# Kernel tuning notes

Hardware: AMD Instinct MI355X
Metric: run time of the kernel (lower is better)

Reference implementation:

```python
import jax, jax.numpy as jnp
import numpy as np

N_BRANCH, N_LAYER = 4, 3
B, T, D_IN = 4, 1024, 32
D_MODEL, D_INNER, D_STATE, D_CONV, DT_RANK = 128, 256, 16, 4, 8
EMBED = 64
MAX_NORM = 10.0  # safe_expmap0 tangent-norm clip
EPS = 1e-7


def setup_inputs() -> dict:
    key = jax.random.key(0)
    ks = jax.random.split(key, 12)
    def nrm(k, shp, s=0.02):
        return s * jax.random.normal(k, shp, dtype=jnp.float32)
    A_init = jnp.log(jnp.arange(1, D_STATE + 1, dtype=jnp.float32))
    return {
        "trend": jax.random.normal(ks[0], (B, T, D_IN), jnp.float32),
        "seasonal_coarse": jax.random.normal(ks[1], (B, T, D_IN), jnp.float32),
        "seasonal_fine": jax.random.normal(ks[2], (B, T, D_IN), jnp.float32),
        "residual": jax.random.normal(ks[3], (B, T, D_IN), jnp.float32),
        "W_ip": nrm(ks[4], (N_BRANCH, D_IN, D_MODEL)),
        "b_ip": jnp.zeros((N_BRANCH, D_MODEL), jnp.float32),
        "W_in": nrm(ks[5], (N_BRANCH, N_LAYER, D_MODEL, 2 * D_INNER)),
        "conv_w": nrm(ks[6], (N_BRANCH, N_LAYER, D_INNER, D_CONV), 0.1),
        "conv_b": jnp.zeros((N_BRANCH, N_LAYER, D_INNER), jnp.float32),
        "W_x": nrm(ks[7], (N_BRANCH, N_LAYER, D_INNER, DT_RANK + 2 * D_STATE)),
        "W_dt": nrm(ks[8], (N_BRANCH, N_LAYER, DT_RANK, D_INNER), 0.1),
        "b_dt": jnp.full((N_BRANCH, N_LAYER, D_INNER), -4.6, jnp.float32),  # softplus ~ 0.01
        "A_log": jnp.broadcast_to(A_init, (N_BRANCH, N_LAYER, D_INNER, D_STATE)),
        "D_param": jnp.ones((N_BRANCH, N_LAYER, D_INNER), jnp.float32),
        "W_out": nrm(ks[9], (N_BRANCH, N_LAYER, D_INNER, D_MODEL)),
        "W_op": nrm(ks[10], (N_BRANCH, D_MODEL, EMBED)),
        "b_op": jnp.zeros((N_BRANCH, EMBED), jnp.float32),
        "eff_scale": jnp.asarray(0.1, jnp.float32),
    }


def _mamba_layer(x, Win, cw, cb, Wx, Wdt, bdt, Alog, Dp, Wout):
    # x: [B, T, d_model]
    Tlen = x.shape[1]
    xz = x @ Win                                   # [B,T,2*di]
    xp, z = jnp.split(xz, 2, axis=-1)
    # causal depthwise conv1d, kernel D_CONV
    xpad = jnp.pad(xp, ((0, 0), (D_CONV - 1, 0), (0, 0)))
    xc = sum(xpad[:, k:k + Tlen, :] * cw[:, k] for k in range(D_CONV))
    xc = jax.nn.silu(xc + cb)                      # [B,T,di]
    dbl = xc @ Wx                                  # [B,T,r+2s]
    dt = jax.nn.softplus(dbl[..., :DT_RANK] @ Wdt + bdt)   # [B,T,di]
    Bm = dbl[..., DT_RANK:DT_RANK + D_STATE]       # [B,T,s]
    Cm = dbl[..., DT_RANK + D_STATE:]              # [B,T,s]
    A = -jnp.exp(Alog)                             # [di,s]
    dA = jnp.exp(dt[..., None] * A)                # [B,T,di,s]
    dBx = (dt * xc)[..., None] * Bm[:, :, None, :] # [B,T,di,s]

    def step(h, inp):
        dA_t, dBx_t, C_t = inp
        h = dA_t * h + dBx_t
        return h, jnp.einsum('bds,bs->bd', h, C_t)

    h0 = jnp.zeros((x.shape[0], D_INNER, D_STATE), x.dtype)
    _, ys = jax.lax.scan(step, h0, (jnp.swapaxes(dA, 0, 1),
                                     jnp.swapaxes(dBx, 0, 1),
                                     jnp.swapaxes(Cm, 0, 1)))
    y = jnp.swapaxes(ys, 0, 1) + Dp * xc
    return (y * jax.nn.silu(z)) @ Wout


def _embed(x, Wip, bip, Wins, cws, cbs, Wxs, Wdts, bdts, Alogs, Dps, Wouts, Wop, bop):
    h = x @ Wip + bip
    for l in range(N_LAYER):
        h = _mamba_layer(h, Wins[l], cws[l], cbs[l], Wxs[l], Wdts[l], bdts[l],
                         Alogs[l], Dps[l], Wouts[l])
    return h.mean(axis=1) @ Wop + bop              # [B, EMBED]


def _expmap0(v):
    # safe expmap0 on Lorentz (k=1): clip tangent norm at MAX_NORM
    n = jnp.linalg.norm(v, axis=-1, keepdims=True)
    nc = jnp.clip(n, EPS, MAX_NORM)
    v = v * (nc / jnp.maximum(n, EPS))
    return jnp.concatenate([jnp.cosh(nc), jnp.sinh(nc) / nc * v], axis=-1)


def _projx(x):
    sp = x[..., 1:]
    t = jnp.sqrt(1.0 + jnp.sum(sp * sp, axis=-1, keepdims=True))
    return jnp.concatenate([t, sp], axis=-1)


def _logmap0(x):
    sp = x[..., 1:]
    t = jnp.maximum(x[..., :1], 1.0 + EPS)
    d = jnp.arccosh(t)
    spn = jnp.maximum(jnp.linalg.norm(sp, axis=-1, keepdims=True), EPS)
    return d * sp / spn


def _forward(trend, seasonal_coarse, seasonal_fine, residual,
             W_ip, b_ip, W_in, conv_w, conv_b, W_x, W_dt, b_dt,
             A_log, D_param, W_out, W_op, b_op, eff_scale):
    xs = [trend, seasonal_coarse, seasonal_fine, residual]
    z_t = [
        _embed(xs[b], W_ip[b], b_ip[b], W_in[b], conv_w[b], conv_b[b], W_x[b],
               W_dt[b], b_dt[b], A_log[b], D_param[b], W_out[b], W_op[b], b_op[b])
        for b in range(N_BRANCH)
    ]
    es = jnp.tanh(eff_scale)
    z_h = [_projx(_expmap0(z * es)) for z in z_t]
    us = [_logmap0(zh) for zh in z_h]
    combined_tangent = us[0] + us[1] + us[2] + us[3]
    combined_h = _projx(_expmap0(combined_tangent * es))
    return (*z_t, *z_h, combined_tangent, combined_h)


def reference(trend, seasonal_coarse, seasonal_fine, residual,
              W_ip, b_ip, W_in, conv_w, conv_b, W_x, W_dt, b_dt,
              A_log, D_param, W_out, W_op, b_op, eff_scale):
    return _forward(trend, seasonal_coarse, seasonal_fine, residual,
                    W_ip, b_ip, W_in, conv_w, conv_b, W_x, W_dt, b_dt,
                    A_log, D_param, W_out, W_op, b_op, eff_scale)
```

## Files before the change

kernel.cpp:

```cpp
#include <hip/hip_runtime.h>
#include <math.h>

#define NBR 4
#define NLAY 3
#define Bk 4
#define Tk 1024
#define DIN 32
#define DMODEL 128
#define DINNER 256
#define DSTATE 16
#define DTRANK 8
#define EMBEDk 64
#define BT (Bk*Tk)
#define EPSF 1e-7f
#define MAXNF 10.0f
#define LCH 64
#define NCH (Tk/LCH)
#define UF 8
#define NWB 320

typedef __bf16 bf16x8 __attribute__((ext_vector_type(8)));
typedef float  f32x4  __attribute__((ext_vector_type(4)));
typedef unsigned short u16x8 __attribute__((ext_vector_type(8)));
typedef unsigned short u16x4 __attribute__((ext_vector_type(4)));

__device__ __forceinline__ float siluf(float x){ return x / (1.f + __expf(-x)); }
__device__ __forceinline__ float softplusf(float x){ return (x > 20.f) ? x : log1pf(__expf(x)); }
__device__ __forceinline__ unsigned short f2b(float x){
    union { float f; unsigned u; } v; v.f = x;
    unsigned r = v.u + 0x7FFF + ((v.u >> 16) & 1);
    return (unsigned short)(r >> 16);
}
__device__ __forceinline__ float b2f(unsigned short u){
    union { unsigned u; float f; } v; v.u = ((unsigned)u) << 16; return v.f;
}

__device__ __forceinline__ void gll16(const void* g, void* l){
    __builtin_amdgcn_global_load_lds(
        (const __attribute__((address_space(1))) unsigned int*)g,
        (__attribute__((address_space(3))) unsigned int*)l,
        16, 0, 0);
}

__device__ __forceinline__ void dA_pow8(float q, int sh, float* dA){
    const float q2 = q * q, q4 = q2 * q2, q8 = q4 * q4;
    const float f = sh ? q8 : 1.0f;
    dA[0] = q * f;       dA[1] = q2 * f;
    dA[2] = q2 * q * f;  dA[3] = q4 * f;
    dA[4] = q4 * q * f;  dA[5] = q4 * q2 * f;
    dA[6] = q4 * q2 * q * f; dA[7] = q8 * f;
}

template<int MODE>
__global__ __launch_bounds__(256) void bgemm_k(
    const unsigned short* __restrict__ Ab, long aBr, int K,
    const unsigned short* __restrict__ Bt, long bBr,
    unsigned short* __restrict__ Cu0, long cu0Br,
    unsigned short* __restrict__ Cu1, long cu1Br,
    float* __restrict__ Cf, long cfBr,
    const float* __restrict__ bias, long biasBr)
{
    const int br = blockIdx.z;
    Ab += (long)br * aBr;
    Bt += (long)br * bBr;
    Cu0 += (long)br * cu0Br;
    if (MODE == 0) Cu1 += (long)br * cu1Br;
    if (MODE == 3) { Cf += (long)br * cfBr; bias += (long)br * biasBr; }
    const int m0 = blockIdx.x * 64, n0 = blockIdx.y * 64;
    __shared__ __align__(16) unsigned short As[8 * 64 * 8];
    __shared__ __align__(16) unsigned short Bs[8 * 64 * 8];
    const int tid = threadIdx.x;
    const int lane = tid & 63, w = tid >> 6;
    const int wm = w >> 1, wn = w & 1;
    const int quad = lane >> 4, l15 = lane & 15;
    f32x4 acc00 = {0,0,0,0}, acc01 = {0,0,0,0}, acc10 = {0,0,0,0}, acc11 = {0,0,0,0};
    for (int kc = 0; kc < K; kc += 64) {
        #pragma unroll
        for (int it = 0; it < 2; ++it) {
            const int kch = w + it * 4;
            gll16(Ab + (long)(m0 + lane) * K + kc + kch * 8, &As[(kch * 64) * 8]);
            gll16(Bt + (long)(n0 + lane) * K + kc + kch * 8, &Bs[(kch * 64) * 8]);
        }
        __syncthreads();
        #pragma unroll
        for (int k0 = 0; k0 < 64; k0 += 32) {
            const int kch = (k0 >> 3) + quad;
            bf16x8 a0 = *(const bf16x8*)&As[(kch * 64 + wm * 32 +      l15) * 8];
            bf16x8 a1 = *(const bf16x8*)&As[(kch * 64 + wm * 32 + 16 + l15) * 8];
            bf16x8 b0 = *(const bf16x8*)&Bs[(kch * 64 + wn * 32 +      l15) * 8];
            bf16x8 b1 = *(const bf16x8*)&Bs[(kch * 64 + wn * 32 + 16 + l15) * 8];
            acc00 = __builtin_amdgcn_mfma_f32_16x16x32_bf16(a0, b0, acc00, 0, 0, 0);
            acc01 = __builtin_amdgcn_mfma_f32_16x16x32_bf16(a0, b1, acc01, 0, 0, 0);
            acc10 = __builtin_amdgcn_mfma_f32_16x16x32_bf16(a1, b0, acc10, 0, 0, 0);
            acc11 = __builtin_amdgcn_mfma_f32_16x16x32_bf16(a1, b1, acc11, 0, 0, 0);
        }
        __syncthreads();
    }
    #pragma unroll
    for (int e = 0; e < 4; ++e) {
        f32x4 a = (e == 0) ? acc00 : (e == 1) ? acc01 : (e == 2) ? acc10 : acc11;
        const int msub = (e >> 1) * 16, nsub = (e & 1) * 16;
        const int col = n0 + wn * 32 + nsub + l15;
        #pragma unroll
        for (int r = 0; r < 4; ++r) {
            const int row = m0 + wm * 32 + msub + quad * 4 + r;
            const float v = a[r];
            if (MODE == 0) {
                if (n0 < 256) Cu0[(long)row * 256 + col] = f2b(v);
                else          Cu1[(long)row * 256 + (col - 256)] = f2b(siluf(v));
            } else {
                if (col < 256)      Cu0[(long)row * 256 + col] = f2b(softplusf(v + bias[col]));
                else if (col < 288) Cf[(long)row * 32 + (col - 256)] = v;
            }
        }
    }
}

__global__ __launch_bounds__(256) void sgemmWT_k(
    const float* __restrict__ Wout, const float* __restrict__ Win,
    const float* __restrict__ Wip, const float* __restrict__ bip,
    const float* __restrict__ Wop,
    unsigned short* __restrict__ WfT, float* __restrict__ Weq,
    float* __restrict__ Wcomb)
{
    const int z = blockIdx.z;
    const int tid = threadIdx.x;
    const int tx = tid & 15, ty = tid >> 4;
    __shared__ float As_[32][68];
    __shared__ float Bs_[32][68];
    float acc[4][4] = {};
    if (z < 8) {
        const int p = z >> 2, br = z & 3;
        const float* A  = Wout + (long)(br * NLAY + p) * DINNER * DMODEL;
        const float* Bw = Win  + (long)(br * NLAY + p + 1) * DMODEL * 512;
        const int m0 = blockIdx.x * 64, n0 = blockIdx.y * 64;
        for (int kc = 0; kc < DMODEL; kc += 32) {
            #pragma unroll
            for (int it = 0; it < 2; ++it) {
                int id = tid + it * 256;
                int r = id >> 3, c4 = (id & 7) << 2;
                float4 v = *(const float4*)(A + (long)(m0 + r) * DMODEL + kc + c4);
                As_[c4+0][r] = v.x; As_[c4+1][r] = v.y; As_[c4+2][r] = v.z; As_[c4+3][r] = v.w;
                int rb = id >> 4, cb = (id & 15) << 2;
                *(float4*)&Bs_[rb][cb] = *(const float4*)(Bw + (long)(kc + rb) * 512 + n0 + cb);
            }
            __syncthreads();
            #pragma unroll
            for (int kk = 0; kk < 32; ++kk) {
                float4 a4 = *(const float4*)&As_[kk][ty << 2];
                float4 b4 = *(const float4*)&Bs_[kk][tx << 2];
                float av[4] = {a4.x, a4.y, a4.z, a4.w};
                float bv[4] = {b4.x, b4.y, b4.z, b4.w};
                #pragma unroll
                for (int i = 0; i < 4; ++i)
                    #pragma unroll
                    for (int j = 0; j < 4; ++j)
                        acc[i][j] = fmaf(av[i], bv[j], acc[i][j]);
            }
            __syncthreads();
        }
        unsigned short* o = WfT + (long)z * 512 * 256;
        const int row0 = m0 + (ty << 2), col = n0 + (tx << 2);
        #pragma unroll
        for (int j = 0; j < 4; ++j) {
            u16x4 v;
            #pragma unroll
            for (int i = 0; i < 4; ++i) v[i] = f2b(acc[i][j]);
            *(u16x4*)(o + (long)(col + j) * 256 + row0) = v;
        }
    } else if (z == 8) {
        const int br = blockIdx.x;
        const float* A  = Wip + (long)br * DIN * DMODEL;
        const float* bp = bip + (long)br * DMODEL;
        const float* Bw = Win + (long)br * NLAY * DMODEL * 512;
        const int n0 = blockIdx.y * 64;
        for (int kc = 0; kc < DMODEL; kc += 32) {
            #pragma unroll
            for (int it = 0; it < 2; ++it) {
                int id = tid + it * 256;
                int r = id >> 3, c4 = (id & 7) << 2;
                float4 v;
                if (r < 32)       v = *(const float4*)(A + (long)r * DMODEL + kc + c4);
                else if (r == 32) v = *(const float4*)(bp + kc + c4);
                else              { v.x = 0.f; v.y = 0.f; v.z = 0.f; v.w = 0.f; }
                As_[c4+0][r] = v.x; As_[c4+1][r] = v.y; As_[c4+2][r] = v.z; As_[c4+3][r] = v.w;
                int rb = id >> 4, cb = (id & 15) << 2;
                *(float4*)&Bs_[rb][cb] = *(const float4*)(Bw + (long)(kc + rb) * 512 + n0 + cb);
            }
            __syncthreads();
            #pragma unroll
            for (int kk = 0; kk < 32; ++kk) {
                float4 a4 = *(const float4*)&As_[kk][ty << 2];
                float4 b4 = *(const float4*)&Bs_[kk][tx << 2];
                float av[4] = {a4.x, a4.y, a4.z, a4.w};
                float bv[4] = {b4.x, b4.y, b4.z, b4.w};
                #pragma unroll
                for (int i = 0; i < 4; ++i)
                    #pragma unroll
                    for (int j = 0; j < 4; ++j)
                        acc[i][j] = fmaf(av[i], bv[j], acc[i][j]);
            }
            __syncthreads();
        }
        float* C = Weq + (long)br * 33 * 512;
        const int col = n0 + (tx << 2);
        #pragma unroll
        for (int i = 0; i < 4; ++i) {
            const int row = (ty << 2) + i;
            if (row < 33) {
                float4 v4; v4.x = acc[i][0]; v4.y = acc[i][1]; v4.z = acc[i][2]; v4.w = acc[i][3];
                *(float4*)(C + (long)row * 512 + col) = v4;
            }
        }
    } else {
        if (blockIdx.y >= 4) return;
        const int br = blockIdx.y;
        const float* A  = Wout + (long)(br * NLAY + 2) * DINNER * DMODEL;
        const float* Bw = Wop  + (long)br * DMODEL * EMBEDk;
        const int m0 = blockIdx.x * 64;
        for (int kc = 0; kc < DMODEL; kc += 32) {
            #pragma unroll
            for (int it = 0; it < 2; ++it) {
                int id = tid + it * 256;
                int r = id >> 3, c4 = (id & 7) << 2;
                float4 v = *(const float4*)(A + (long)(m0 + r) * DMODEL + kc + c4);
                As_[c4+0][r] = v.x; As_[c4+1][r] = v.y; As_[c4+2][r] = v.z; As_[c4+3][r] = v.w;
                int rb = id >> 4, cb = (id & 15) << 2;
                if (cb < 64)
                    *(float4*)&Bs_[rb][cb] = *(const float4*)(Bw + (long)(kc + rb) * EMBEDk + cb);
            }
            __syncthreads();
            #pragma unroll
            for (int kk = 0; kk < 32; ++kk) {
                float4 a4 = *(const float4*)&As_[kk][ty << 2];
                float4 b4 = *(const float4*)&Bs_[kk][tx << 2];
                float av[4] = {a4.x, a4.y, a4.z, a4.w};
                float bv[4] = {b4.x, b4.y, b4.z, b4.w};
                #pragma unroll
                for (int i = 0; i < 4; ++i)
                    #pragma unroll
                    for (int j = 0; j < 4; ++j)
                        acc[i][j] = fmaf(av[i], bv[j], acc[i][j]);
            }
            __syncthreads();
        }
        float* C = Wcomb + (long)br * DINNER * EMBEDk;
        const int col = tx << 2;
        #pragma unroll
        for (int i = 0; i < 4; ++i) {
            const int row = m0 + (ty << 2) + i;
            float4 v4; v4.x = acc[i][0]; v4.y = acc[i][1]; v4.z = acc[i][2]; v4.w = acc[i][3];
            *(float4*)(C + (long)row * EMBEDk + col) = v4;
        }
    }
}

__global__ __launch_bounds__(256) void prepC_k(
    const float* __restrict__ Wx, const float* __restrict__ Wdt,
    unsigned short* __restrict__ o)
{
    const int n = blockIdx.x, bl = blockIdx.y;
    const int k = threadIdx.x;
    const float* WxP = Wx + (long)bl * DINNER * 40;
    float v;
    if (n < 256) {
        const float* WdtP = Wdt + (long)bl * DTRANK * DINNER;
        float s = 0.f;
        #pragma unroll
        for (int r = 0; r < 8; ++r) s = fmaf(WxP[k * 40 + r], WdtP[r * DINNER + n], s);
        v = s;
    } else if (n < 288) {
        v = WxP[k * 40 + 8 + (n - 256)];
    } else {
        v = 0.f;
    }
    o[(long)bl * NWB * DINNER + (long)n * DINNER + k] = f2b(v);
}

__global__ __launch_bounds__(256) void xgemm0_k(
    const float* __restrict__ A0, const float* __restrict__ A1,
    const float* __restrict__ A2, const float* __restrict__ A3,
    const float* __restrict__ Weq,
    unsigned short* __restrict__ zb, unsigned short* __restrict__ xpb)
{
    const int br = blockIdx.z;
    const float* A = (br == 1) ? A1 : (br == 2) ? A2 : (br == 3) ? A3 : A0;
    const float* W = Weq + (long)br * 33 * 512;
    unsigned short* Cz = zb + (long)br * BT * DINNER;
    unsigned short* Cb = xpb + (long)br * BT * DINNER;
    const int m0 = blockIdx.x * 64, n0 = blockIdx.y * 64;
    __shared__ float As_[32][68];
    __shared__ float Bs_[32][68];
    const int tid = threadIdx.x;
    const int tx = tid & 15, ty = tid >> 4;
    float acc[4][4] = {};
    {
        #pragma unroll
        for (int it = 0; it < 2; ++it) {
            int id = tid + it * 256;
            int r = id >> 3, c4 = (id & 7) << 2;
            float4 v = *(const float4*)(A + (long)(m0 + r) * DIN + c4);
            As_[c4+0][r] = v.x; As_[c4+1][r] = v.y; As_[c4+2][r] = v.z; As_[c4+3][r] = v.w;
            int rb = id >> 4, cb = (id & 15) << 2;
            *(float4*)&Bs_[rb][cb] = *(const float4*)(W + (long)rb * 512 + n0 + cb);
        }
        __syncthreads();
        #pragma unroll
        for (int kk = 0; kk < 32; ++kk) {
            float4 a4 = *(const float4*)&As_[kk][ty << 2];
            float4 b4 = *(const float4*)&Bs_[kk][tx << 2];
            float av[4] = {a4.x, a4.y, a4.z, a4.w};
            float bv[4] = {b4.x, b4.y, b4.z, b4.w};
            #pragma unroll
            for (int i = 0; i < 4; ++i)
                #pragma unroll
                for (int j = 0; j < 4; ++j)
                    acc[i][j] = fmaf(av[i], bv[j], acc[i][j]);
        }
    }
    const int col = n0 + (tx << 2);
    float be[4];
    #pragma unroll
    for (int j = 0; j < 4; ++j) be[j] = W[32 * 512 + col + j];
    #pragma unroll
    for (int i = 0; i < 4; ++i) {
        const int row = m0 + (ty << 2) + i;
        #pragma unroll
        for (int j = 0; j < 4; ++j) {
            const float v = acc[i][j] + be[j];
            if (n0 < 256) Cb[(long)row * 256 + col + j] = f2b(v);
            else          Cz[(long)row * 256 + (col - 256 + j)] = f2b(siluf(v));
        }
    }
}

__global__ __launch_bounds__(256) void conv_k(
    const unsigned short* __restrict__ xp, const float* __restrict__ cw,
    const float* __restrict__ cb, unsigned short* __restrict__ xcb, int layer)
{
    const int br = blockIdx.y;
    const long base = (long)br * BT * DINNER;
    const long idx8 = ((long)blockIdx.x * 256 + threadIdx.x) * 8;
    const int d0 = (int)(idx8 & (DINNER - 1));
    const long row = idx8 >> 8;
    const int t = (int)(row & (Tk - 1));
    const float* cwp = cw + ((long)(br * NLAY + layer) * DINNER + d0) * 4;
    const float* cbp = cb + (long)(br * NLAY + layer) * DINNER + d0;
    u16x8 in[4];
    #pragma unroll
    for (int k = 0; k < 4; ++k) {
        const int tt = t + k - 3;
        if (tt >= 0) {
            in[k] = *(const u16x8*)(xp + base + idx8 + (long)(k - 3) * DINNER);
        } else {
            #pragma unroll
            for (int j = 0; j < 8; ++j) in[k][j] = 0;
        }
    }
    u16x8 o;
    #pragma unroll
    for (int j = 0; j < 8; ++j) {
        float acc = cbp[j];
        #pragma unroll
        for (int k = 0; k < 4; ++k)
            acc = fmaf(b2f(in[k][j]), cwp[j * 4 + k], acc);
        o[j] = f2b(siluf(acc));
    }
    *(u16x8*)(xcb + base + idx8) = o;
}

__global__ __launch_bounds__(512) void scan1_k(
    const unsigned short* __restrict__ dtb, const unsigned short* __restrict__ xcb,
    const float* __restrict__ bcb, const float* __restrict__ Alog,
    float* __restrict__ recbuf, int layer)
{
    const int c = blockIdx.x, b = blockIdx.y, br = blockIdx.z;
    const int tid = threadIdx.x;
    const int d = tid >> 1, sh = tid & 1, s0 = sh << 3;
    const float* Ap = Alog + ((long)(br * NLAY + layer) * DINNER + d) * DSTATE + s0;
    float Aa[8]; bool pw = true;
    #pragma unroll
    for (int k = 0; k < 8; ++k) {
        Aa[k] = -__expf(Ap[k]);
        pw = pw && (fabsf(Aa[k] + (float)(s0 + k + 1)) < 1e-3f);
    }
    const long rbase = (long)br * BT + (long)b * Tk + (long)c * LCH;
    const unsigned short* dtp = dtb + rbase * DINNER + d;
    const unsigned short* xcp = xcb + rbase * DINNER + d;
    __shared__ float bcs[LCH * 32];
    ((float4*)bcs)[tid] = ((const float4*)(bcb + rbase * 32))[tid];
    float dtc[UF], xcc[UF];
    #pragma unroll
    for (int u = 0; u < UF; ++u) {
        dtc[u] = b2f(dtp[(long)u * DINNER]);
        xcc[u] = b2f(xcp[(long)u * DINNER]);
    }
    __syncthreads();
    float h[8];
    #pragma unroll
    for (int k = 0; k < 8; ++k) h[k] = 0.f;
    float sumdt = 0.f;
    for (int base = 0; base < LCH; base += UF) {
        const int nb = (base + UF < LCH) ? base + UF : base;
        float dtn[UF], xcn[UF];
        #pragma unroll
        for (int u = 0; u < UF; ++u) {
            dtn[u] = b2f(dtp[(long)(nb + u) * DINNER]);
            xcn[u] = b2f(xcp[(long)(nb + u) * DINNER]);
        }
        #pragma unroll
        for (int u = 0; u < UF; ++u) {
            const int t = base + u;
            const float dtv = dtc[u];
            const float dtxc = dtv * xcc[u];
            sumdt += dtv;
            float dA[8];
            if (pw) dA_pow8(__expf(-dtv), sh, dA);
            else {
                #pragma unroll
                for (int k = 0; k < 8; ++k) dA[k] = __expf(dtv * Aa[k]);
            }
            const float* bcT = bcs + t * 32 + s0;
            #pragma unroll
            for (int k = 0; k < 8; ++k)
                h[k] = fmaf(dA[k], h[k], dtxc * bcT[k]);
        }
        #pragma unroll
        for (int u = 0; u < UF; ++u) { dtc[u] = dtn[u]; xcc[u] = xcn[u]; }
    }
    float* sb = recbuf + (((long)(br * 4 + b) * (NCH - 1) + c) * 17) * 256 + d;
    #pragma unroll
    for (int k = 0; k < 8; ++k) sb[(s0 + k) * 256] = h[k];
    if (!sh) sb[16 * 256] = sumdt;
}

__global__ __launch_bounds__(512) void scan3_k(
    const unsigned short* __restrict__ dtb, const unsigned short* __restrict__ xcb,
    const float* __restrict__ bcb, const unsigned short* __restrict__ zb,
    const float* __restrict__ Alog, const float* __restrict__ Dpar,
    const float* __restrict__ recbuf, unsigned short* __restrict__ yzb, int layer)
{
    const int c = blockIdx.x, b = blockIdx.y, br = blockIdx.z;
    const int tid = threadIdx.x;
    const int d = tid >> 1, sh = tid & 1, s0 = sh << 3;
    const float* Ap = Alog + ((long)(br * NLAY + layer) * DINNER + d) * DSTATE + s0;
    float Aa[8]; bool pw = true;
    #pragma unroll
    for (int k = 0; k < 8; ++k) {
        Aa[k] = -__expf(Ap[k]);
        pw = pw && (fabsf(Aa[k] + (float)(s0 + k + 1)) < 1e-3f);
    }
    float h[8];
    #pragma unroll
    for (int k = 0; k < 8; ++k) h[k] = 0.f;
    if (c > 0) {
        const float* recB = recbuf + ((long)(br * 4 + b) * (NCH - 1)) * 17 * 256 + d;
        float rh[8], rs;
        #pragma unroll
        for (int k = 0; k < 8; ++k) rh[k] = recB[(s0 + k) * 256];
        rs = recB[16 * 256];
        for (int cc = 0; cc < c; ++cc) {
            float nh[8], ns = 0.f;
            if (cc + 1 < c) {
                const float* r2 = recB + (long)(cc + 1) * 17 * 256;
                #pragma unroll
                for (int k = 0; k < 8; ++k) nh[k] = r2[(s0 + k) * 256];
                ns = r2[16 * 256];
            } else {
                #pragma unroll
                for (int k = 0; k < 8; ++k) nh[k] = 0.f;
            }
            float P[8];
            if (pw) dA_pow8(__expf(-rs), sh, P);
            else {
                #pragma unroll
                for (int k = 0; k < 8; ++k) P[k] = __expf(rs * Aa[k]);
            }
            #pragma unroll
            for (int k = 0; k < 8; ++k) h[k] = fmaf(h[k], P[k], rh[k]);
            #pragma unroll
            for (int k = 0; k < 8; ++k) rh[k] = nh[k];
            rs = ns;
        }
    }
    const float Dp = Dpar[(br * NLAY + layer) * DINNER + d];
    const long rbase = (long)br * BT + (long)b * Tk + (long)c * LCH;
    const unsigned short* dtp = dtb + rbase * DINNER + d;
    const unsigned short* xcp = xcb + rbase * DINNER + d;
    const unsigned short* zp  = zb  + rbase * DINNER + d;
    unsigned short* yp = yzb + rbase * DINNER + d;
    __shared__ float bcs[LCH * 32];
    ((float4*)bcs)[tid] = ((const float4*)(bcb + rbase * 32))[tid];
    float dtc[UF], xcc[UF], zc[UF];
    #pragma unroll
    for (int u = 0; u < UF; ++u) {
        dtc[u] = b2f(dtp[(long)u * DINNER]);
        xcc[u] = b2f(xcp[(long)u * DINNER]);
        zc[u]  = b2f(zp[(long)u * DINNER]);
    }
    __syncthreads();
    for (int base = 0; base < LCH; base += UF) {
        const int nb = (base + UF < LCH) ? base + UF : base;
        float dtn[UF], xcn[UF], zn[UF];
        #pragma unroll
        for (int u = 0; u < UF; ++u) {
            dtn[u] = b2f(dtp[(long)(nb + u) * DINNER]);
            xcn[u] = b2f(xcp[(long)(nb + u) * DINNER]);
            zn[u]  = b2f(zp[(long)(nb + u) * DINNER]);
        }
        #pragma unroll
        for (int u = 0; u < UF; ++u) {
            const int t = base + u;
            const float dtv = dtc[u], xcv = xcc[u];
            const float dtxc = dtv * xcv;
            float dA[8];
            if (pw) dA_pow8(__expf(-dtv), sh, dA);
            else {
                #pragma unroll
                for (int k = 0; k < 8; ++k) dA[k] = __expf(dtv * Aa[k]);
            }
            const float* bcT = bcs + t * 32 + s0;
            #pragma unroll
            for (int k = 0; k < 8; ++k)
                h[k] = fmaf(dA[k], h[k], dtxc * bcT[k]);
            float y0 = 0.f, y1 = 0.f;
            const float* cT = bcs + t * 32 + 16 + s0;
            #pragma unroll
            for (int k = 0; k < 8; k += 2) {
                y0 = fmaf(h[k+0], cT[k+0], y0);
                y1 = fmaf(h[k+1], cT[k+1], y1);
            }
            const float yp_ = y0 + y1;
            const float ytot = yp_ + __shfl_xor(yp_, 1);
            if (!sh) {
                const float y = ytot + Dp * xcv;
                yp[(long)t * DINNER] = f2b(y * zc[u]);
            }
        }
        #pragma unroll
        for (int u = 0; u < UF; ++u) { dtc[u] = dtn[u]; xcc[u] = xcn[u]; zc[u] = zn[u]; }
    }
}

__global__ __launch_bounds__(256) void csum1_k(
    const unsigned short* __restrict__ yz, float* __restrict__ part)
{
    const int ch = blockIdx.x, brb = blockIdx.y;
    const int br = brb >> 2, b = brb & 3;
    const long rbase = (long)br * BT + (long)b * Tk + (long)ch * 128;
    const int tid = threadIdx.x;
    const int cg = tid & 31;
    const int ro = tid >> 5;
    const unsigned short* p = yz + (rbase + ro) * DINNER + cg * 8;
    float acc[8] = {0,0,0,0,0,0,0,0};
    for (int it = 0; it < 16; ++it) {
        u16x8 v = *(const u16x8*)(p + (long)it * 8 * DINNER);
        #pragma unroll
        for (int j = 0; j < 8; ++j) acc[j] += b2f(v[j]);
    }
    __shared__ float sm[8][256];
    #pragma unroll
    for (int j = 0; j < 8; ++j) sm[ro][cg * 8 + j] = acc[j];
    __syncthreads();
    float s = 0.f;
    #pragma unroll
    for (int r = 0; r < 8; ++r) s += sm[r][tid];
    part[((long)brb * 8 + ch) * 256 + tid] = s;
}

__global__ __launch_bounds__(256) void csum2_k(
    const float* __restrict__ part, const float* __restrict__ Wcomb,
    const float* __restrict__ bop, float* __restrict__ outzt)
{
    const int brb = blockIdx.x, br = brb >> 2;
    const int tid = threadIdx.x;
    __shared__ float vm[256];
    __shared__ float red[4][64];
    float s = 0.f;
    #pragma unroll
    for (int ch = 0; ch < 8; ++ch) s += part[((long)brb * 8 + ch) * 256 + tid];
    vm[tid] = s * (1.0f / Tk);
    __syncthreads();
    const float* Wc = Wcomb + (long)br * DINNER * EMBEDk;
    const int col = tid & 63, seg = tid >> 6;
    float a = 0.f;
    #pragma unroll 8
    for (int k = seg * 64; k < seg * 64 + 64; ++k)
        a = fmaf(vm[k], Wc[(long)k * EMBEDk + col], a);
    red[seg][col] = a;
    __syncthreads();
    if (tid < 64)
        outzt[brb * EMBEDk + tid] =
            red[0][tid] + red[1][tid] + red[2][tid] + red[3][tid] + bop[br * EMBEDk + tid];
}

__global__ __launch_bounds__(64) void final_k(
    const float* __restrict__ zt, float* __restrict__ out, const float* __restrict__ eff)
{
    const float es = tanhf(eff[0]);
    __shared__ float us[NBR][Bk][EMBEDk];
    const int t = threadIdx.x;
    if (t < 16) {
        const int br = t >> 2, b = t & 3;
        const float* z = zt + br * (Bk * EMBEDk) + b * EMBEDk;
        float n2 = 0.f;
        for (int e = 0; e < EMBEDk; ++e) { float v = z[e] * es; n2 = fmaf(v, v, n2); }
        const float n  = sqrtf(n2);
        const float nc = fminf(fmaxf(n, EPSF), MAXNF);
        const float sc = nc / fmaxf(n, EPSF);
        const float sh = sinhf(nc) / nc;
        const float fac = es * sc * sh;
        float* zh = out + 1024 + br * (Bk * (EMBEDk + 1)) + b * (EMBEDk + 1);
        float sp2 = 0.f;
        for (int e = 0; e < EMBEDk; ++e) {
            float spv = z[e] * fac;
            sp2 = fmaf(spv, spv, sp2);
            zh[1 + e] = spv;
            us[br][b][e] = spv;
        }
        const float t0 = sqrtf(1.f + sp2);
        zh[0] = t0;
        const float dd  = acoshf(fmaxf(t0, 1.f + EPSF));
        const float spn = fmaxf(sqrtf(sp2), EPSF);
        const float rr  = dd / spn;
        for (int e = 0; e < EMBEDk; ++e) us[br][b][e] *= rr;
    }
    __syncthreads();
    if (t < 4) {
        const int b = t;
        float ct[EMBEDk];
        float* cto = out + 2064 + b * EMBEDk;
        for (int e = 0; e < EMBEDk; ++e) {
            float v = us[0][b][e] + us[1][b][e] + us[2][b][e] + us[3][b][e];
            ct[e] = v; cto[e] = v;
        }
        float n2 = 0.f;
        for (int e = 0; e < EMBEDk; ++e) { float v = ct[e] * es; n2 = fmaf(v, v, n2); }
        const float n  = sqrtf(n2);
        const float nc = fminf(fmaxf(n, EPSF), MAXNF);
        const float sc = nc / fmaxf(n, EPSF);
        const float sh = sinhf(nc) / nc;
        const float fac = es * sc * sh;
        float* ch = out + 2320 + b * (EMBEDk + 1);
        float sp2 = 0.f;
        for (int e = 0; e < EMBEDk; ++e) {
            float spv = ct[e] * fac;
            sp2 = fmaf(spv, spv, sp2);
            ch[1 + e] = spv;
        }
        ch[0] = sqrtf(1.f + sp2);
    }
}

extern "C" void kernel_launch(void* const* d_in, const int* in_sizes, int n_in,
                              void* d_out, int out_size, void* d_ws, size_t ws_size,
                              hipStream_t stream)
{
    const float* X0 = (const float*)d_in[0];
    const float* X1 = (const float*)d_in[1];
    const float* X2 = (const float*)d_in[2];
    const float* X3 = (const float*)d_in[3];
    const float* W_ip   = (const float*)d_in[4];
    const float* b_ip   = (const float*)d_in[5];
    const float* W_in   = (const float*)d_in[6];
    const float* conv_w = (const float*)d_in[7];
    const float* conv_b = (const float*)d_in[8];
    const float* W_x    = (const float*)d_in[9];
    const float* W_dt   = (const float*)d_in[10];
    const float* b_dt   = (const float*)d_in[11];
    const float* A_log  = (const float*)d_in[12];
    const float* D_par  = (const float*)d_in[13];
    const float* W_out  = (const float*)d_in[14];
    const float* W_op   = (const float*)d_in[15];
    const float* b_op   = (const float*)d_in[16];
    const float* eff    = (const float*)d_in[17];
    float* out = (float*)d_out;
    float* ws  = (float*)d_ws;

    float* buf_bc = ws;
    float* part   = buf_bc + (long)NBR * BT * 32;
    float* recbuf = part + 32768;
    float* Weq    = recbuf + (long)16 * (NCH - 1) * 17 * 256;
    float* Wcomb  = Weq + 4 * 33 * 512;
    unsigned short* xp_bf = (unsigned short*)(Wcomb + 4 * 256 * 64);
    unsigned short* xc_bf = xp_bf + (long)NBR * BT * DINNER;
    unsigned short* z_bf  = xc_bf + (long)NBR * BT * DINNER;
    unsigned short* dt_bf = z_bf  + (long)NBR * BT * DINNER;
    unsigned short* yz_bf = dt_bf + (long)NBR * BT * DINNER;
    unsigned short* WfT   = yz_bf + (long)NBR * BT * DINNER;
    unsigned short* WcT   = WfT   + (long)8 * 512 * DINNER;

    prepC_k<<<dim3(NWB, NBR * NLAY), 256, 0, stream>>>(W_x, W_dt, WcT);
    sgemmWT_k<<<dim3(4, 8, 10), 256, 0, stream>>>(
        W_out, W_in, W_ip, b_ip, W_op, WfT, Weq, Wcomb);

    xgemm0_k<<<dim3(BT / 64, 8, NBR), 256, 0, stream>>>(
        X0, X1, X2, X3, Weq, z_bf, xp_bf);

    for (int l = 0; l < NLAY; ++l) {
        if (l > 0) {
            bgemm_k<0><<<dim3(BT / 64, 8, NBR), 256, 0, stream>>>(
                yz_bf, (long)BT * DINNER, DINNER,
                WfT + (long)(l - 1) * 4 * 512 * DINNER, (long)512 * DINNER,
                xp_bf, (long)BT * DINNER,
                z_bf, (long)BT * DINNER,
                nullptr, 0, nullptr, 0);
        }
        conv_k<<<dim3((BT * DINNER) / (256 * 8), NBR), 256, 0, stream>>>(
            xp_bf, conv_w, conv_b, xc_bf, l);
        bgemm_k<3><<<dim3(BT / 64, NWB / 64, NBR), 256, 0, stream>>>(
            xc_bf, (long)BT * DINNER, DINNER,
            WcT + (long)l * NWB * DINNER, (long)NLAY * NWB * DINNER,
            dt_bf, (long)BT * DINNER,
            nullptr, 0,
            buf_bc, (long)BT * 32,
            b_dt + l * DINNER, (long)NLAY * DINNER);
        scan1_k<<<dim3(NCH - 1, Bk, NBR), 512, 0, stream>>>(
            dt_bf, xc_bf, buf_bc, A_log, recbuf, l);
        scan3_k<<<dim3(NCH, Bk, NBR), 512, 0, stream>>>(
            dt_bf, xc_bf, buf_bc, z_bf, A_log, D_par, recbuf, yz_bf, l);
    }

    csum1_k<<<dim3(8, 16), 256, 0, stream>>>(yz_bf, part);
    csum2_k<<<16, 256, 0, stream>>>(part, Wcomb, b_op, out);
    final_k<<<1, 64, 0, stream>>>(out, out, eff);
}
```

Measured before the change: 424.0 us.

## Widen bgemm N-tile, fold weight prep into sgemmWT, fuse final time-sum into scan

The bf16 MFMA GEMM now computes a 64x128 tile per block, doubling B-tile reuse and halving the grid in the N direction. NWB is padded to 384 so the x-projection GEMM needs three wide tiles. The separate prepC kernel is merged into sgemmWT as extra z-slices, removing a launch. The last layer's scan now accumulates y*z per chunk straight into partial sums, which drops the yz store and the csum1 kernel. The trade-offs are more register pressure in the GEMM and some wasted padded columns.

After: 419.9 us (median of 2 runs). No clear change (-1.0%).

```diff
diff --git a/kernel.cpp b/kernel.cpp
--- a/kernel.cpp
+++ b/kernel.cpp
@@ -17,7 +17,7 @@
 #define LCH 64
 #define NCH (Tk/LCH)
 #define UF 8
-#define NWB 320
+#define NWB 384
 
 typedef __bf16 bf16x8 __attribute__((ext_vector_type(8)));
 typedef float  f32x4  __attribute__((ext_vector_type(4)));
@@ -66,20 +66,30 @@
     Cu0 += (long)br * cu0Br;
     if (MODE == 0) Cu1 += (long)br * cu1Br;
     if (MODE == 3) { Cf += (long)br * cfBr; bias += (long)br * biasBr; }
-    const int m0 = blockIdx.x * 64, n0 = blockIdx.y * 64;
+    const int m0 = blockIdx.x * 64, n0 = blockIdx.y * 128;
     __shared__ __align__(16) unsigned short As[8 * 64 * 8];
-    __shared__ __align__(16) unsigned short Bs[8 * 64 * 8];
+    __shared__ __align__(16) unsigned short Bs[8 * 128 * 8];
     const int tid = threadIdx.x;
     const int lane = tid & 63, w = tid >> 6;
     const int wm = w >> 1, wn = w & 1;
     const int quad = lane >> 4, l15 = lane & 15;
-    f32x4 acc00 = {0,0,0,0}, acc01 = {0,0,0,0}, acc10 = {0,0,0,0}, acc11 = {0,0,0,0};
+    f32x4 acc[2][4];
+    #pragma unroll
+    for (int nt = 0; nt < 2; ++nt)
+        #pragma unroll
+        for (int e = 0; e < 4; ++e) { f32x4 zz = {0,0,0,0}; acc[nt][e] = zz; }
     for (int kc = 0; kc < K; kc += 64) {
         #pragma unroll
         for (int it = 0; it < 2; ++it) {
             const int kch = w + it * 4;
             gll16(Ab + (long)(m0 + lane) * K + kc + kch * 8, &As[(kch * 64) * 8]);
-            gll16(Bt + (long)(n0 + lane) * K + kc + kch * 8, &Bs[(kch * 64) * 8]);
+        }
+        #pragma unroll
+        for (int it = 0; it < 4; ++it) {
+            const int ub = w * 256 + it * 64;
+            const int u = ub + lane;
+            const int kch = u >> 7, nrow = u & 127;
+            gll16(Bt + (long)(n0 + nrow) * K + kc + kch * 8, &Bs[ub * 8]);
         }
         __syncthreads();
         #pragma unroll
@@ -87,41 +97,83 @@
             const int kch = (k0 >> 3) + quad;
             bf16x8 a0 = *(const bf16x8*)&As[(kch * 64 + wm * 32 +      l15) * 8];
             bf16x8 a1 = *(const bf16x8*)&As[(kch * 64 + wm * 32 + 16 + l15) * 8];
-            bf16x8 b0 = *(const bf16x8*)&Bs[(kch * 64 + wn * 32 +      l15) * 8];
-            bf16x8 b1 = *(const bf16x8*)&Bs[(kch * 64 + wn * 32 + 16 + l15) * 8];
-            acc00 = __builtin_amdgcn_mfma_f32_16x16x32_bf16(a0, b0, acc00, 0, 0, 0);
-            acc01 = __builtin_amdgcn_mfma_f32_16x16x32_bf16(a0, b1, acc01, 0, 0, 0);
-            acc10 = __builtin_amdgcn_mfma_f32_16x16x32_bf16(a1, b0, acc10, 0, 0, 0);
-            acc11 = __builtin_amdgcn_mfma_f32_16x16x32_bf16(a1, b1, acc11, 0, 0, 0);
+            #pragma unroll
+            for (int nt = 0; nt < 2; ++nt) {
+                bf16x8 b0 = *(const bf16x8*)&Bs[(kch * 128 + nt * 64 + wn * 32 +      l15) * 8];
+                bf16x8 b1 = *(const bf16x8*)&Bs[(kch * 128 + nt * 64 + wn * 32 + 16 + l15) * 8];
+                acc[nt][0] = __builtin_amdgcn_mfma_f32_16x16x32_bf16(a0, b0, acc[nt][0], 0, 0, 0);
+                acc[nt][1] = __builtin_amdgcn_mfma_f32_16x16x32_bf16(a0, b1, acc[nt][1], 0, 0, 0);
+                acc[nt][2] = __builtin_amdgcn_mfma_f32_16x16x32_bf16(a1, b0, acc[nt][2], 0, 0, 0);
+                acc[nt][3] = __builtin_amdgcn_mfma_f32_16x16x32_bf16(a1, b1, acc[nt][3], 0, 0, 0);
+            }
         }
         __syncthreads();
     }
     #pragma unroll
-    for (int e = 0; e < 4; ++e) {
-        f32x4 a = (e == 0) ? acc00 : (e == 1) ? acc01 : (e == 2) ? acc10 : acc11;
-        const int msub = (e >> 1) * 16, nsub = (e & 1) * 16;
-        const int col = n0 + wn * 32 + nsub + l15;
-        #pragma unroll
-        for (int r = 0; r < 4; ++r) {
-            const int row = m0 + wm * 32 + msub + quad * 4 + r;
-            const float v = a[r];
-            if (MODE == 0) {
-                if (n0 < 256) Cu0[(long)row * 256 + col] = f2b(v);
-                else          Cu1[(long)row * 256 + (col - 256)] = f2b(siluf(v));
-            } else {
-                if (col < 256)      Cu0[(long)row * 256 + col] = f2b(softplusf(v + bias[col]));
-                else if (col < 288) Cf[(long)row * 32 + (col - 256)] = v;
-            }
-        }
-    }
+    for (int nt = 0; nt < 2; ++nt) {
+        #pragma unroll
+        for (int e = 0; e < 4; ++e) {
+            const f32x4 a = acc[nt][e];
+            const int msub = (e >> 1) * 16, nsub = (e & 1) * 16;
+            const int col = n0 + nt * 64 + wn * 32 + nsub + l15;
+            #pragma unroll
+            for (int r = 0; r < 4; ++r) {
+                const int row = m0 + wm * 32 + msub + quad * 4 + r;
+                const float v = a[r];
+                if (MODE == 0) {
+                    if (col < 256) Cu0[(long)row * 256 + col] = f2b(v);
+                    else           Cu1[(long)row * 256 + (col - 256)] = f2b(siluf(v));
+                } else {
+                    if (col < 256)      Cu0[(long)row * 256 + col] = f2b(softplusf(v + bias[col]));
+                    else if (col < 288) Cf[(long)row * 32 + (col - 256)] = v;
+                }
+            }
+        }
+    }
+}
+
+__global__ __launch_bounds__(256) void conv_k(
+    const unsigned short* __restrict__ xp, const float* __restrict__ cw,
+    const float* __restrict__ cb, unsigned short* __restrict__ xcb, int layer)
+{
+    const int br = blockIdx.y;
+    const long base = (long)br * BT * DINNER;
+    const long idx8 = ((long)blockIdx.x * 256 + threadIdx.x) * 8;
+    const int d0 = (int)(idx8 & (DINNER - 1));
+    const long row = idx8 >> 8;
+    const int t = (int)(row & (Tk - 1));
+    const float* cwp = cw + ((long)(br * NLAY + layer) * DINNER + d0) * 4;
+    const float* cbp = cb + (long)(br * NLAY + layer) * DINNER + d0;
+    u16x8 in[4];
+    #pragma unroll
+    for (int k = 0; k < 4; ++k) {
+        const int tt = t + k - 3;
+        if (tt >= 0) {
+            in[k] = *(const u16x8*)(xp + base + idx8 + (long)(k - 3) * DINNER);
+        } else {
+            #pragma unroll
+            for (int j = 0; j < 8; ++j) in[k][j] = 0;
+        }
+    }
+    u16x8 o;
+    #pragma unroll
+    for (int j = 0; j < 8; ++j) {
+        float acc = cbp[j];
+        #pragma unroll
+        for (int k = 0; k < 4; ++k)
+            acc = fmaf(b2f(in[k][j]), cwp[j * 4 + k], acc);
+        o[j] = f2b(siluf(acc));
+    }
+    *(u16x8*)(xcb + base + idx8) = o;
 }
 
 __global__ __launch_bounds__(256) void sgemmWT_k(
     const float* __restrict__ Wout, const float* __restrict__ Win,
     const float* __restrict__ Wip, const float* __restrict__ bip,
     const float* __restrict__ Wop,
+    const float* __restrict__ Wx, const float* __restrict__ Wdt,
     unsigned short* __restrict__ WfT, float* __restrict__ Weq,
-    float* __restrict__ Wcomb)
+    float* __restrict__ Wcomb, unsigned short* __restrict__ WcT)
 {
     const int z = blockIdx.z;
     const int tid = threadIdx.x;
@@ -212,7 +264,7 @@
                 *(float4*)(C + (long)row * 512 + col) = v4;
             }
         }
-    } else {
+    } else if (z == 9) {
         if (blockIdx.y >= 4) return;
         const int br = blockIdx.y;
         const float* A  = Wout + (long)(br * NLAY + 2) * DINNER * DMODEL;
@@ -252,29 +304,29 @@
             float4 v4; v4.x = acc[i][0]; v4.y = acc[i][1]; v4.z = acc[i][2]; v4.w = acc[i][3];
             *(float4*)(C + (long)row * EMBEDk + col) = v4;
         }
-    }
-}
-
-__global__ __launch_bounds__(256) void prepC_k(
-    const float* __restrict__ Wx, const float* __restrict__ Wdt,
-    unsigned short* __restrict__ o)
-{
-    const int n = blockIdx.x, bl = blockIdx.y;
-    const int k = threadIdx.x;
-    const float* WxP = Wx + (long)bl * DINNER * 40;
-    float v;
-    if (n < 256) {
+    } else {
+        const int bl = z - 10;
+        const int base = (blockIdx.x * 8 + blockIdx.y) * 12;
+        const float* WxP = Wx + (long)bl * DINNER * 40;
         const float* WdtP = Wdt + (long)bl * DTRANK * DINNER;
-        float s = 0.f;
-        #pragma unroll
-        for (int r = 0; r < 8; ++r) s = fmaf(WxP[k * 40 + r], WdtP[r * DINNER + n], s);
-        v = s;
-    } else if (n < 288) {
-        v = WxP[k * 40 + 8 + (n - 256)];
-    } else {
-        v = 0.f;
-    }
-    o[(long)bl * NWB * DINNER + (long)n * DINNER + k] = f2b(v);
+        unsigned short* o = WcT + (long)bl * NWB * DINNER;
+        #pragma unroll
+        for (int i = 0; i < 12; ++i) {
+            const int n = base + i;
+            float v;
+            if (n < 256) {
+                float s = 0.f;
+                #pragma unroll
+                for (int r = 0; r < 8; ++r) s = fmaf(WxP[tid * 40 + r], WdtP[r * DINNER + n], s);
+                v = s;
+            } else if (n < 288) {
+                v = WxP[tid * 40 + 8 + (n - 256)];
+            } else {
+                v = 0.f;
+            }
+            o[(long)n * DINNER + tid] = f2b(v);
+        }
+    }
 }
 
 __global__ __launch_bounds__(256) void xgemm0_k(
@@ -334,41 +386,6 @@
     }
 }
 
-__global__ __launch_bounds__(256) void conv_k(
-    const unsigned short* __restrict__ xp, const float* __restrict__ cw,
-    const float* __restrict__ cb, unsigned short* __restrict__ xcb, int layer)
-{
-    const int br = blockIdx.y;
-    const long base = (long)br * BT * DINNER;
-    const long idx8 = ((long)blockIdx.x * 256 + threadIdx.x) * 8;
-    const int d0 = (int)(idx8 & (DINNER - 1));
-    const long row = idx8 >> 8;
-    const int t = (int)(row & (Tk - 1));
-    const float* cwp = cw + ((long)(br * NLAY + layer) * DINNER + d0) * 4;
-    const float* cbp = cb + (long)(br * NLAY + layer) * DINNER + d0;
-    u16x8 in[4];
-    #pragma unroll
-    for (int k = 0; k < 4; ++k) {
-        const int tt = t + k - 3;
-        if (tt >= 0) {
-            in[k] = *(const u16x8*)(xp + base + idx8 + (long)(k - 3) * DINNER);
-        } else {
-            #pragma unroll
-            for (int j = 0; j < 8; ++j) in[k][j] = 0;
-        }
-    }
-    u16x8 o;
-    #pragma unroll
-    for (int j = 0; j < 8; ++j) {
-        float acc = cbp[j];
-        #pragma unroll
-        for (int k = 0; k < 4; ++k)
-            acc = fmaf(b2f(in[k][j]), cwp[j * 4 + k], acc);
-        o[j] = f2b(siluf(acc));
-    }
-    *(u16x8*)(xcb + base + idx8) = o;
-}
-
 __global__ __launch_bounds__(512) void scan1_k(
     const unsigned short* __restrict__ dtb, const unsigned short* __restrict__ xcb,
     const float* __restrict__ bcb, const float* __restrict__ Alog,
@@ -434,11 +451,13 @@
     if (!sh) sb[16 * 256] = sumdt;
 }
 
+template<int LAST>
 __global__ __launch_bounds__(512) void scan3_k(
     const unsigned short* __restrict__ dtb, const unsigned short* __restrict__ xcb,
     const float* __restrict__ bcb, const unsigned short* __restrict__ zb,
     const float* __restrict__ Alog, const float* __restrict__ Dpar,
-    const float* __restrict__ recbuf, unsigned short* __restrict__ yzb, int layer)
+    const float* __restrict__ recbuf, unsigned short* __restrict__ yzb,
+    float* __restrict__ part, int layer)
 {
     const int c = blockIdx.x, b = blockIdx.y, br = blockIdx.z;
     const int tid = threadIdx.x;
@@ -499,6 +518,7 @@
         zc[u]  = b2f(zp[(long)u * DINNER]);
     }
     __syncthreads();
+    float ysum = 0.f;
     for (int base = 0; base < LCH; base += UF) {
         const int nb = (base + UF < LCH) ? base + UF : base;
         float dtn[UF], xcn[UF], zn[UF];
@@ -532,40 +552,18 @@
             }
             const float yp_ = y0 + y1;
             const float ytot = yp_ + __shfl_xor(yp_, 1);
-            if (!sh) {
-                const float y = ytot + Dp * xcv;
+            const float y = ytot + Dp * xcv;
+            if (LAST) {
+                ysum += y * zc[u];
+            } else if (!sh) {
                 yp[(long)t * DINNER] = f2b(y * zc[u]);
             }
         }
         #pragma unroll
         for (int u = 0; u < UF; ++u) { dtc[u] = dtn[u]; xcc[u] = xcn[u]; zc[u] = zn[u]; }
     }
-}
-
-__global__ __launch_bounds__(256) void csum1_k(
-    const unsigned short* __restrict__ yz, float* __restrict__ part)
-{
-    const int ch = blockIdx.x, brb = blockIdx.y;
-    const int br = brb >> 2, b = brb & 3;
-    const long rbase = (long)br * BT + (long)b * Tk + (long)ch * 128;
-    const int tid = threadIdx.x;
-    const int cg = tid & 31;
-    const int ro = tid >> 5;
-    const unsigned short* p = yz + (rbase + ro) * DINNER + cg * 8;
-    float acc[8] = {0,0,0,0,0,0,0,0};
-    for (int it = 0; it < 16; ++it) {
-        u16x8 v = *(const u16x8*)(p + (long)it * 8 * DINNER);
-        #pragma unroll
-        for (int j = 0; j < 8; ++j) acc[j] += b2f(v[j]);
-    }
-    __shared__ float sm[8][256];
-    #pragma unroll
-    for (int j = 0; j < 8; ++j) sm[ro][cg * 8 + j] = acc[j];
-    __syncthreads();
-    float s = 0.f;
-    #pragma unroll
-    for (int r = 0; r < 8; ++r) s += sm[r][tid];
-    part[((long)brb * 8 + ch) * 256 + tid] = s;
+    if (LAST && !sh)
+        part[((long)(br * 4 + b) * 16 + c) * 256 + d] = ysum;
 }
 
 __global__ __launch_bounds__(256) void csum2_k(
@@ -578,7 +576,7 @@
     __shared__ float red[4][64];
     float s = 0.f;
     #pragma unroll
-    for (int ch = 0; ch < 8; ++ch) s += part[((long)brb * 8 + ch) * 256 + tid];
+    for (int ch = 0; ch < 16; ++ch) s += part[((long)brb * 16 + ch) * 256 + tid];
     vm[tid] = s * (1.0f / Tk);
     __syncthreads();
     const float* Wc = Wcomb + (long)br * DINNER * EMBEDk;
@@ -679,7 +677,7 @@
 
     float* buf_bc = ws;
     float* part   = buf_bc + (long)NBR * BT * 32;
-    float* recbuf = part + 32768;
+    float* recbuf = part + 65536;
     float* Weq    = recbuf + (long)16 * (NCH - 1) * 17 * 256;
     float* Wcomb  = Weq + 4 * 33 * 512;
     unsigned short* xp_bf = (unsigned short*)(Wcomb + 4 * 256 * 64);
@@ -690,16 +688,15 @@
     unsigned short* WfT   = yz_bf + (long)NBR * BT * DINNER;
     unsigned short* WcT   = WfT   + (long)8 * 512 * DINNER;
 
-    prepC_k<<<dim3(NWB, NBR * NLAY), 256, 0, stream>>>(W_x, W_dt, WcT);
-    sgemmWT_k<<<dim3(4, 8, 10), 256, 0, stream>>>(
-        W_out, W_in, W_ip, b_ip, W_op, WfT, Weq, Wcomb);
+    sgemmWT_k<<<dim3(4, 8, 22), 256, 0, stream>>>(
+        W_out, W_in, W_ip, b_ip, W_op, W_x, W_dt, WfT, Weq, Wcomb, WcT);
 
     xgemm0_k<<<dim3(BT / 64, 8, NBR), 256, 0, stream>>>(
         X0, X1, X2, X3, Weq, z_bf, xp_bf);
 
     for (int l = 0; l < NLAY; ++l) {
         if (l > 0) {
-            bgemm_k<0><<<dim3(BT / 64, 8, NBR), 256, 0, stream>>>(
+            bgemm_k<0><<<dim3(BT / 64, 4, NBR), 256, 0, stream>>>(
                 yz_bf, (long)BT * DINNER, DINNER,
                 WfT + (long)(l - 1) * 4 * 512 * DINNER, (long)512 * DINNER,
                 xp_bf, (long)BT * DINNER,
@@ -708,7 +705,7 @@
         }
         conv_k<<<dim3((BT * DINNER) / (256 * 8), NBR), 256, 0, stream>>>(
             xp_bf, conv_w, conv_b, xc_bf, l);
-        bgemm_k<3><<<dim3(BT / 64, NWB / 64, NBR), 256, 0, stream>>>(
+        bgemm_k<3><<<dim3(BT / 64, 3, NBR), 256, 0, stream>>>(
             xc_bf, (long)BT * DINNER, DINNER,
             WcT + (long)l * NWB * DINNER, (long)NLAY * NWB * DINNER,
             dt_bf, (long)BT * DINNER,
@@ -717,11 +714,15 @@
             b_dt + l * DINNER, (long)NLAY * DINNER);
         scan1_k<<<dim3(NCH - 1, Bk, NBR), 512, 0, stream>>>(
             dt_bf, xc_bf, buf_bc, A_log, recbuf, l);
-        scan3_k<<<dim3(NCH, Bk, NBR), 512, 0, stream>>>(
-            dt_bf, xc_bf, buf_bc, z_bf, A_log, D_par, recbuf, yz_bf, l);
-    }
-
-    csum1_k<<<dim3(8, 16), 256, 0, stream>>>(yz_bf, part);
+        if (l < NLAY - 1) {
+            scan3_k<0><<<dim3(NCH, Bk, NBR), 512, 0, stream>>>(
+                dt_bf, xc_bf, buf_bc, z_bf, A_log, D_par, recbuf, yz_bf, nullptr, l);
+        } else {
+            scan3_k<1><<<dim3(NCH, Bk, NBR), 512, 0, stream>>>(
+                dt_bf, xc_bf, buf_bc, z_bf, A_log, D_par, recbuf, yz_bf, part, l);
+        }
+    }
+
     csum2_k<<<16, 256, 0, stream>>>(part, Wcomb, b_op, out);
     final_k<<<1, 64, 0, stream>>>(out, out, eff);
 }
```
